# Kernel optimization log

Hardware: AMD Instinct MI355X
Metric: run time of the kernel (lower is better)

## Reference

```python
import jax, jax.numpy as jnp
import numpy as np

H = 32  # hidden_size
D = 512  # input_size


def _lstm_layer(x_tbd, Wih, Whh, b):
    """Single PyTorch-convention LSTM layer.
    x_tbd: [T, B, Din]; Wih: [4H, Din]; Whh: [4H, H]; b: [4H] (b_ih + b_hh).
    Gate order (PyTorch): i, f, g, o. Returns outputs [T, B, H]."""
    T, B, _ = x_tbd.shape
    # Precompute the input contribution for all timesteps at once.
    xg = jnp.einsum('tbd,gd->tbg', x_tbd, Wih) + b  # [T, B, 4H]

    def step(carry, xg_t):
        h, c = carry
        gates = xg_t + h @ Whh.T  # [B, 4H]
        i, f, g, o = jnp.split(gates, 4, axis=-1)
        i = jax.nn.sigmoid(i)
        f = jax.nn.sigmoid(f)
        g = jnp.tanh(g)
        o = jax.nn.sigmoid(o)
        c = f * c + i * g
        h = o * jnp.tanh(c)
        return (h, c), h

    h0 = jnp.zeros((B, H), dtype=x_tbd.dtype)
    c0 = jnp.zeros((B, H), dtype=x_tbd.dtype)
    _, ys = jax.lax.scan(step, (h0, c0), xg)
    return ys  # [T, B, H]


def setup_inputs() -> dict:
    key = jax.random.key(0)
    ks = jax.random.split(key, 9)
    s = 1.0 / np.sqrt(H)  # PyTorch LSTM init: U(-1/sqrt(H), 1/sqrt(H))
    u = lambda k, shape: jax.random.uniform(k, shape, jnp.float32, -s, s)
    return {
        'x': jax.random.normal(ks[0], (64, 1024, D), dtype=jnp.float32),
        'Wih0': u(ks[1], (4 * H, D)),
        'Whh0': u(ks[2], (4 * H, H)),
        'bih0': u(ks[3], (4 * H,)),
        'bhh0': u(ks[4], (4 * H,)),
        'Wih1': u(ks[5], (4 * H, H)),
        'Whh1': u(ks[6], (4 * H, H)),
        'bih1': u(ks[7], (4 * H,)),
        'bhh1': u(ks[8], (4 * H,)),
    }


def reference(x, Wih0, Whh0, bih0, bhh0, Wih1, Whh1, bih1, bhh1):
    # x: [B, T, D] (batch_first) -> scan over time axis
    x_tbd = jnp.transpose(x, (1, 0, 2))  # [T, B, D]
    y0 = _lstm_layer(x_tbd, Wih0, Whh0, bih0 + bhh0)  # [T, B, H]
    y1 = _lstm_layer(y0, Wih1, Whh1, bih1 + bhh1)     # [T, B, H]
    return jnp.transpose(y1, (1, 0, 2))  # [B, T, H]
```

## Files before the change

### kernel.cpp

```cpp
#include <hip/hip_runtime.h>
#include <stdint.h>


#define TT 1024
#define BB 64
#define DD 512
#define HH 32
#define GG 128

typedef _Float16 h2v __attribute__((ext_vector_type(2)));
typedef __fp16 pk2 __attribute__((ext_vector_type(2)));
typedef int int2v __attribute__((ext_vector_type(2)));
typedef _Float16 f16x8 __attribute__((ext_vector_type(8)));
typedef float f32x4 __attribute__((ext_vector_type(4)));

__device__ __forceinline__ uint32_t pack2(float lo, float hi) {
  pk2 p = __builtin_amdgcn_cvt_pkrtz(lo, hi);
  return __builtin_bit_cast(uint32_t, p);
}
__device__ __forceinline__ float dot2(uint32_t a, uint32_t b, float acc) {
  return __builtin_amdgcn_fdot2(__builtin_bit_cast(h2v, a),
                                __builtin_bit_cast(h2v, b), acc, false);
}
__device__ __forceinline__ float fast_rcp(float x) { return __builtin_amdgcn_rcpf(x); }
__device__ __forceinline__ float sigm(float s) { return fast_rcp(1.f + __expf(-s)); }
__device__ __forceinline__ float fast_tanh(float x) {
  return fmaf(2.f, fast_rcp(1.f + __expf(-2.f * x)), -1.f);
}
__device__ __forceinline__ float act_sel(float s, bool ist) {
  float z = ist ? s + s : s;
  float r = fast_rcp(1.f + __expf(-z));
  return ist ? fmaf(2.f, r, -1.f) : r;
}

__device__ __forceinline__ float partner32(float x) {
  int xi = __builtin_bit_cast(int, x);
#if __has_builtin(__builtin_amdgcn_permlane32_swap)
  int2v r = __builtin_amdgcn_permlane32_swap(xi, xi, false, false);
  return __builtin_bit_cast(float, r.x ^ r.y ^ xi);
#else
  int a = xi, b = xi;
  asm("v_permlane32_swap_b32 %0, %1" : "+v"(a), "+v"(b));
  return __builtin_bit_cast(float, a ^ b ^ xi);
#endif
}

__device__ __forceinline__ float xor1_dpp(float x) {
  int xi = __builtin_bit_cast(int, x);
  int r = __builtin_amdgcn_update_dpp(xi, xi, 0xB1, 0xF, 0xF, true);
  return __builtin_bit_cast(float, r);
}

__global__ __launch_bounds__(256) void xg_gemm_mfma(const float* __restrict__ x,
                                                    const float* __restrict__ W,
                                                    const float* __restrict__ bih,
                                                    const float* __restrict__ bhh,
                                                    float* __restrict__ outp) {
  __shared__ _Float16 lxs[128][40];
  __shared__ _Float16 lws[128][40];
  const int tid = threadIdx.x;
  const int m0 = blockIdx.x * 128;
  const int sr = tid >> 1;
  const int sk = (tid & 1) * 16;
  const int w = tid >> 6;
  const int wm = (w >> 1) * 64;
  const int wn = (w & 1) * 64;
  const int lane = tid & 63;
  const int lr = lane & 15;
  const int lk = (lane >> 4) * 8;

  f32x4 acc[4][4];
#pragma unroll
  for (int i = 0; i < 4; ++i)
#pragma unroll
    for (int j = 0; j < 4; ++j) acc[i][j] = (f32x4){0.f, 0.f, 0.f, 0.f};

  for (int k0 = 0; k0 < DD; k0 += 32) {
#pragma unroll
    for (int c = 0; c < 4; ++c) {
      const float4 xv = *(const float4*)(x + (size_t)(m0 + sr) * DD + k0 + sk + c * 4);
      uint2 px;
      px.x = pack2(xv.x, xv.y);
      px.y = pack2(xv.z, xv.w);
      *(uint2*)&lxs[sr][sk + c * 4] = px;
      const float4 wv = *(const float4*)(W + (size_t)sr * DD + k0 + sk + c * 4);
      uint2 pw;
      pw.x = pack2(wv.x, wv.y);
      pw.y = pack2(wv.z, wv.w);
      *(uint2*)&lws[sr][sk + c * 4] = pw;
    }
    __syncthreads();
    f16x8 af[4], bf[4];
#pragma unroll
    for (int s = 0; s < 4; ++s) {
      af[s] = *(const f16x8*)&lxs[wm + s * 16 + lr][lk];
      bf[s] = *(const f16x8*)&lws[wn + s * 16 + lr][lk];
    }
#pragma unroll
    for (int mi = 0; mi < 4; ++mi)
#pragma unroll
      for (int ni = 0; ni < 4; ++ni)
        acc[mi][ni] = __builtin_amdgcn_mfma_f32_16x16x32_f16(af[mi], bf[ni],
                                                             acc[mi][ni], 0, 0, 0);
    __syncthreads();
  }
  const int rq = (lane >> 4) * 4;
#pragma unroll
  for (int ni = 0; ni < 4; ++ni) {
    const int g = wn + ni * 16 + lr;
    const float bsum = bih[g] + bhh[g];
#pragma unroll
    for (int mi = 0; mi < 4; ++mi) {
      const int mbase = m0 + wm + mi * 16 + rq;
#pragma unroll
      for (int q = 0; q < 4; ++q)
        outp[(size_t)(mbase + q) * GG + g] = acc[mi][ni][q] + bsum;
    }
  }
}

__global__ __launch_bounds__(64)
__attribute__((amdgpu_waves_per_eu(1)))
void lstm_scan(const float* __restrict__ xg,
               const float* __restrict__ Whh0,
               const float* __restrict__ Wih1,
               const float* __restrict__ Whh1,
               const float* __restrict__ bih1,
               const float* __restrict__ bhh1,
               float* __restrict__ out) {
  const int l = threadIdx.x;
  const int j = l & 31;
  const int hi = l >> 5;
  const int b = blockIdx.x;
  const int gA = j + 64 * hi;
  const int gB = gA + 32;

  uint32_t w0A[16], w0B[16], wiA[16], whA[16], wiB[16], whB[16];
#pragma unroll
  for (int q = 0; q < 8; ++q) {
    float4 a = *(const float4*)(Whh0 + (size_t)gA * HH + q * 4);
    float4 c = *(const float4*)(Whh0 + (size_t)gB * HH + q * 4);
    w0A[2 * q] = pack2(a.x, a.y); w0A[2 * q + 1] = pack2(a.z, a.w);
    w0B[2 * q] = pack2(c.x, c.y); w0B[2 * q + 1] = pack2(c.z, c.w);
    float4 d = *(const float4*)(Wih1 + (size_t)gA * HH + q * 4);
    float4 e = *(const float4*)(Wih1 + (size_t)gB * HH + q * 4);
    wiA[2 * q] = pack2(d.x, d.y); wiA[2 * q + 1] = pack2(d.z, d.w);
    wiB[2 * q] = pack2(e.x, e.y); wiB[2 * q + 1] = pack2(e.z, e.w);
    float4 f = *(const float4*)(Whh1 + (size_t)gA * HH + q * 4);
    float4 g = *(const float4*)(Whh1 + (size_t)gB * HH + q * 4);
    whA[2 * q] = pack2(f.x, f.y); whA[2 * q + 1] = pack2(f.z, f.w);
    whB[2 * q] = pack2(g.x, g.y); whB[2 * q + 1] = pack2(g.z, g.w);
  }
#pragma unroll
  for (int k = 0; k < 16; ++k) {
    asm volatile("" : "+v"(w0A[k]));
    asm volatile("" : "+v"(w0B[k]));
    asm volatile("" : "+v"(wiA[k]));
    asm volatile("" : "+v"(wiB[k]));
    asm volatile("" : "+v"(whA[k]));
    asm volatile("" : "+v"(whB[k]));
  }
  const float b1A = bih1[gA] + bhh1[gA];
  const float b1B = bih1[gB] + bhh1[gB];

  uint32_t h0p[16], h1p[16];
#pragma unroll
  for (int k = 0; k < 16; ++k) { h0p[k] = 0u; h1p[k] = 0u; }
  float c0 = 0.f, c1 = 0.f;

  const float* xgp = xg + (size_t)b * TT * GG;
  float* outp = out + (size_t)b * TT * HH;

  float xA[4], xB[4];
#pragma unroll
  for (int u = 0; u < 4; ++u) {
    xA[u] = xgp[u * GG + gA];
    xB[u] = xgp[u * GG + gB];
  }

  for (int tb = 0; tb < TT; tb += 4) {
#pragma unroll
    for (int u = 0; u < 4; ++u) {
      const int t = tb + u;
      float sA0 = xA[u], sB0 = xB[u];
      const int tp = (t + 4 < TT) ? (t + 4) : (TT - 1);
      xA[u] = xgp[(size_t)tp * GG + gA];
      xB[u] = xgp[(size_t)tp * GG + gB];
      float pA = 0.f, pB = 0.f;
#pragma unroll
      for (int k = 0; k < 16; k += 2) {
        sA0 = dot2(w0A[k], h0p[k], sA0);
        pA  = dot2(w0A[k + 1], h0p[k + 1], pA);
        sB0 = dot2(w0B[k], h0p[k], sB0);
        pB  = dot2(w0B[k + 1], h0p[k + 1], pB);
      }
      sA0 += pA; sB0 += pB;
      float sA1 = b1A, sB1 = b1B, qA = 0.f, qB = 0.f;
#pragma unroll
      for (int k = 0; k < 16; k += 2) {
        sA1 = dot2(wiA[k], h0p[k], sA1);
        qA  = dot2(wiA[k + 1], h0p[k + 1], qA);
        sB1 = dot2(wiB[k], h0p[k], sB1);
        qB  = dot2(wiB[k + 1], h0p[k + 1], qB);
        sA1 = dot2(whA[k], h1p[k], sA1);
        qA  = dot2(whA[k + 1], h1p[k + 1], qA);
        sB1 = dot2(whB[k], h1p[k], sB1);
        qB  = dot2(whB[k + 1], h1p[k + 1], qB);
      }
      sA1 += qA; sB1 += qB;
      {
        float aA = act_sel(sA0, hi != 0);
        float aB = sigm(sB0);
        float pAx = partner32(aA);
        float pBx = partner32(aB);
        float gi = hi ? pAx : aA;
        float gf = hi ? pBx : aB;
        float gg = hi ? aA : pAx;
        float go = hi ? aB : pBx;
        c0 = fmaf(gf, c0, gi * gg);
        float h = go * fast_tanh(c0);
        float oth = xor1_dpp(h);
        float lo = (j & 1) ? oth : h;
        float hh = (j & 1) ? h : oth;
        uint32_t pk = pack2(lo, hh);
#pragma unroll
        for (int m = 0; m < 16; ++m)
          h0p[m] = (uint32_t)__builtin_amdgcn_readlane((int)pk, 2 * m);
      }
      if (t > 0) {
        float aA = act_sel(sA1, hi != 0);
        float aB = sigm(sB1);
        float pAx = partner32(aA);
        float pBx = partner32(aB);
        float gi = hi ? pAx : aA;
        float gf = hi ? pBx : aB;
        float gg = hi ? aA : pAx;
        float go = hi ? aB : pBx;
        c1 = fmaf(gf, c1, gi * gg);
        float h = go * fast_tanh(c1);
        if (!hi) outp[(size_t)(t - 1) * HH + j] = h;
        float oth = xor1_dpp(h);
        float lo = (j & 1) ? oth : h;
        float hh = (j & 1) ? h : oth;
        uint32_t pk = pack2(lo, hh);
#pragma unroll
        for (int m = 0; m < 16; ++m)
          h1p[m] = (uint32_t)__builtin_amdgcn_readlane((int)pk, 2 * m);
      }
    }
  }
  {
    float sA1 = b1A, sB1 = b1B, qA = 0.f, qB = 0.f;
#pragma unroll
    for (int k = 0; k < 16; k += 2) {
      sA1 = dot2(wiA[k], h0p[k], sA1);
      qA  = dot2(wiA[k + 1], h0p[k + 1], qA);
      sB1 = dot2(wiB[k], h0p[k], sB1);
      qB  = dot2(wiB[k + 1], h0p[k + 1], qB);
      sA1 = dot2(whA[k], h1p[k], sA1);
      qA  = dot2(whA[k + 1], h1p[k + 1], qA);
      sB1 = dot2(whB[k], h1p[k], sB1);
      qB  = dot2(whB[k + 1], h1p[k + 1], qB);
    }
    sA1 += qA; sB1 += qB;
    float aA = act_sel(sA1, hi != 0);
    float aB = sigm(sB1);
    float pAx = partner32(aA);
    float pBx = partner32(aB);
    float gi = hi ? pAx : aA;
    float gf = hi ? pBx : aB;
    float gg = hi ? aA : pAx;
    float go = hi ? aB : pBx;
    c1 = fmaf(gf, c1, gi * gg);
    float h = go * fast_tanh(c1);
    if (!hi) outp[(size_t)(TT - 1) * HH + j] = h;
  }
}

extern "C" void kernel_launch(void* const* d_in, const int* in_sizes, int n_in,
                              void* d_out, int out_size, void* d_ws, size_t ws_size,
                              hipStream_t stream) {
  const float* x = (const float*)d_in[0];
  const float* Wih0 = (const float*)d_in[1];
  const float* Whh0 = (const float*)d_in[2];
  const float* bih0 = (const float*)d_in[3];
  const float* bhh0 = (const float*)d_in[4];
  const float* Wih1 = (const float*)d_in[5];
  const float* Whh1 = (const float*)d_in[6];
  const float* bih1 = (const float*)d_in[7];
  const float* bhh1 = (const float*)d_in[8];
  float* out = (float*)d_out;
  float* xg = (float*)d_ws;

  xg_gemm_mfma<<<dim3((BB * TT) / 128), dim3(256), 0, stream>>>(x, Wih0, bih0, bhh0, xg);
  lstm_scan<<<dim3(BB), dim3(64), 0, stream>>>(xg, Whh0, Wih1, Whh1, bih1, bhh1, out);
}
```

Measured before the change: 497.2 us.

## Split LSTM layers into producer/consumer waves with an LDS ring buffer

The single-wave recurrent scan is split across two wavefronts per block. Wave 0 runs layer 0 and precomputes part of layer 1's input projection. Wave 1 runs layer 1, reading h0 and the partial sums from a shared-memory ring buffer, with spin-wait counters for flow control. The aim is to overlap the two layers' serial dependency chains so each per-step critical path gets shorter. This adds LDS traffic, polling with s_sleep, and relies on volatile counters plus a block fence for memory ordering.

```diff
diff --git a/kernel.cpp b/kernel.cpp
--- a/kernel.cpp
+++ b/kernel.cpp
@@ -7,6 +7,7 @@
 #define DD 512
 #define HH 32
 #define GG 128
+#define RINGD 8
 
 typedef _Float16 h2v __attribute__((ext_vector_type(2)));
 typedef __fp16 pk2 __attribute__((ext_vector_type(2)));
@@ -119,96 +120,80 @@
   }
 }
 
-__global__ __launch_bounds__(64)
-__attribute__((amdgpu_waves_per_eu(1)))
-void lstm_scan(const float* __restrict__ xg,
-               const float* __restrict__ Whh0,
-               const float* __restrict__ Wih1,
-               const float* __restrict__ Whh1,
-               const float* __restrict__ bih1,
-               const float* __restrict__ bhh1,
-               float* __restrict__ out) {
-  const int l = threadIdx.x;
+__global__ __launch_bounds__(128)
+void lstm_scan2(const float* __restrict__ xg,
+                const float* __restrict__ Whh0,
+                const float* __restrict__ Wih1,
+                const float* __restrict__ Whh1,
+                const float* __restrict__ bih1,
+                const float* __restrict__ bhh1,
+                float* __restrict__ out) {
+  __shared__ alignas(16) uint32_t h0ring[RINGD][16];
+  __shared__ alignas(16) float pring[RINGD][64];
+  __shared__ volatile int prodCnt;
+  __shared__ volatile int consCnt;
+
+  const int tid = threadIdx.x;
+  const int wid = tid >> 6;
+  const int l = tid & 63;
   const int j = l & 31;
   const int hi = l >> 5;
   const int b = blockIdx.x;
   const int gA = j + 64 * hi;
   const int gB = gA + 32;
 
-  uint32_t w0A[16], w0B[16], wiA[16], whA[16], wiB[16], whB[16];
-#pragma unroll
-  for (int q = 0; q < 8; ++q) {
-    float4 a = *(const float4*)(Whh0 + (size_t)gA * HH + q * 4);
-    float4 c = *(const float4*)(Whh0 + (size_t)gB * HH + q * 4);
-    w0A[2 * q] = pack2(a.x, a.y); w0A[2 * q + 1] = pack2(a.z, a.w);
-    w0B[2 * q] = pack2(c.x, c.y); w0B[2 * q + 1] = pack2(c.z, c.w);
-    float4 d = *(const float4*)(Wih1 + (size_t)gA * HH + q * 4);
-    float4 e = *(const float4*)(Wih1 + (size_t)gB * HH + q * 4);
-    wiA[2 * q] = pack2(d.x, d.y); wiA[2 * q + 1] = pack2(d.z, d.w);
-    wiB[2 * q] = pack2(e.x, e.y); wiB[2 * q + 1] = pack2(e.z, e.w);
-    float4 f = *(const float4*)(Whh1 + (size_t)gA * HH + q * 4);
-    float4 g = *(const float4*)(Whh1 + (size_t)gB * HH + q * 4);
-    whA[2 * q] = pack2(f.x, f.y); whA[2 * q + 1] = pack2(f.z, f.w);
-    whB[2 * q] = pack2(g.x, g.y); whB[2 * q + 1] = pack2(g.z, g.w);
-  }
-#pragma unroll
-  for (int k = 0; k < 16; ++k) {
-    asm volatile("" : "+v"(w0A[k]));
-    asm volatile("" : "+v"(w0B[k]));
-    asm volatile("" : "+v"(wiA[k]));
-    asm volatile("" : "+v"(wiB[k]));
-    asm volatile("" : "+v"(whA[k]));
-    asm volatile("" : "+v"(whB[k]));
-  }
-  const float b1A = bih1[gA] + bhh1[gA];
-  const float b1B = bih1[gB] + bhh1[gB];
-
-  uint32_t h0p[16], h1p[16];
-#pragma unroll
-  for (int k = 0; k < 16; ++k) { h0p[k] = 0u; h1p[k] = 0u; }
-  float c0 = 0.f, c1 = 0.f;
-
-  const float* xgp = xg + (size_t)b * TT * GG;
-  float* outp = out + (size_t)b * TT * HH;
-
-  float xA[4], xB[4];
-#pragma unroll
-  for (int u = 0; u < 4; ++u) {
-    xA[u] = xgp[u * GG + gA];
-    xB[u] = xgp[u * GG + gB];
-  }
-
-  for (int tb = 0; tb < TT; tb += 4) {
+  if (tid == 0) { prodCnt = 0; consCnt = 0; }
+  __syncthreads();
+
+  if (wid == 0) {
+    uint32_t w0A[16], w0B[16], wiA[16];
+#pragma unroll
+    for (int q = 0; q < 8; ++q) {
+      float4 a = *(const float4*)(Whh0 + (size_t)gA * HH + q * 4);
+      float4 c = *(const float4*)(Whh0 + (size_t)gB * HH + q * 4);
+      w0A[2 * q] = pack2(a.x, a.y); w0A[2 * q + 1] = pack2(a.z, a.w);
+      w0B[2 * q] = pack2(c.x, c.y); w0B[2 * q + 1] = pack2(c.z, c.w);
+      float4 d = *(const float4*)(Wih1 + (size_t)gA * HH + q * 4);
+      wiA[2 * q] = pack2(d.x, d.y); wiA[2 * q + 1] = pack2(d.z, d.w);
+    }
+    uint32_t h0p[16];
+#pragma unroll
+    for (int k = 0; k < 16; ++k) h0p[k] = 0u;
+    float c0 = 0.f;
+
+    const float* xgp = xg + (size_t)b * TT * GG;
+    float xA[4], xB[4];
 #pragma unroll
     for (int u = 0; u < 4; ++u) {
-      const int t = tb + u;
-      float sA0 = xA[u], sB0 = xB[u];
-      const int tp = (t + 4 < TT) ? (t + 4) : (TT - 1);
-      xA[u] = xgp[(size_t)tp * GG + gA];
-      xB[u] = xgp[(size_t)tp * GG + gB];
-      float pA = 0.f, pB = 0.f;
-#pragma unroll
-      for (int k = 0; k < 16; k += 2) {
-        sA0 = dot2(w0A[k], h0p[k], sA0);
-        pA  = dot2(w0A[k + 1], h0p[k + 1], pA);
-        sB0 = dot2(w0B[k], h0p[k], sB0);
-        pB  = dot2(w0B[k + 1], h0p[k + 1], pB);
-      }
-      sA0 += pA; sB0 += pB;
-      float sA1 = b1A, sB1 = b1B, qA = 0.f, qB = 0.f;
-#pragma unroll
-      for (int k = 0; k < 16; k += 2) {
-        sA1 = dot2(wiA[k], h0p[k], sA1);
-        qA  = dot2(wiA[k + 1], h0p[k + 1], qA);
-        sB1 = dot2(wiB[k], h0p[k], sB1);
-        qB  = dot2(wiB[k + 1], h0p[k + 1], qB);
-        sA1 = dot2(whA[k], h1p[k], sA1);
-        qA  = dot2(whA[k + 1], h1p[k + 1], qA);
-        sB1 = dot2(whB[k], h1p[k], sB1);
-        qB  = dot2(whB[k + 1], h1p[k + 1], qB);
-      }
-      sA1 += qA; sB1 += qB;
-      {
+      xA[u] = xgp[u * GG + gA];
+      xB[u] = xgp[u * GG + gB];
+    }
+    const bool wrt = (!hi) && ((j & 1) == 0);
+    int cachedCons = 0;
+
+    for (int tb = 0; tb < TT; tb += 4) {
+#pragma unroll
+      for (int u = 0; u < 4; ++u) {
+        const int t = tb + u;
+        if (t - cachedCons >= RINGD) {
+          do {
+            __builtin_amdgcn_s_sleep(1);
+            cachedCons = consCnt;
+          } while (t - cachedCons >= RINGD);
+        }
+        float sA0 = xA[u], sB0 = xB[u];
+        const int tp = (t + 4 < TT) ? (t + 4) : (TT - 1);
+        xA[u] = xgp[(size_t)tp * GG + gA];
+        xB[u] = xgp[(size_t)tp * GG + gB];
+        float pA = 0.f, pB = 0.f;
+#pragma unroll
+        for (int k = 0; k < 16; k += 2) {
+          sA0 = dot2(w0A[k], h0p[k], sA0);
+          pA  = dot2(w0A[k + 1], h0p[k + 1], pA);
+          sB0 = dot2(w0B[k], h0p[k], sB0);
+          pB  = dot2(w0B[k + 1], h0p[k + 1], pB);
+        }
+        sA0 += pA; sB0 += pB;
         float aA = act_sel(sA0, hi != 0);
         float aB = sigm(sB0);
         float pAx = partner32(aA);
@@ -226,54 +211,87 @@
 #pragma unroll
         for (int m = 0; m < 16; ++m)
           h0p[m] = (uint32_t)__builtin_amdgcn_readlane((int)pk, 2 * m);
+        float pp0 = 0.f, pp1 = 0.f;
+#pragma unroll
+        for (int k = 0; k < 16; k += 2) {
+          pp0 = dot2(wiA[k], h0p[k], pp0);
+          pp1 = dot2(wiA[k + 1], h0p[k + 1], pp1);
+        }
+        if (wrt) h0ring[t & (RINGD - 1)][j >> 1] = pk;
+        pring[t & (RINGD - 1)][l] = pp0 + pp1;
+        __threadfence_block();
+        if (l == 0) prodCnt = t + 1;
       }
-      if (t > 0) {
-        float aA = act_sel(sA1, hi != 0);
-        float aB = sigm(sB1);
-        float pAx = partner32(aA);
-        float pBx = partner32(aB);
-        float gi = hi ? pAx : aA;
-        float gf = hi ? pBx : aB;
-        float gg = hi ? aA : pAx;
-        float go = hi ? aB : pBx;
-        c1 = fmaf(gf, c1, gi * gg);
-        float h = go * fast_tanh(c1);
-        if (!hi) outp[(size_t)(t - 1) * HH + j] = h;
-        float oth = xor1_dpp(h);
-        float lo = (j & 1) ? oth : h;
-        float hh = (j & 1) ? h : oth;
-        uint32_t pk = pack2(lo, hh);
-#pragma unroll
-        for (int m = 0; m < 16; ++m)
-          h1p[m] = (uint32_t)__builtin_amdgcn_readlane((int)pk, 2 * m);
+    }
+  } else {
+    uint32_t wiB[16], whA[16], whB[16];
+#pragma unroll
+    for (int q = 0; q < 8; ++q) {
+      float4 e = *(const float4*)(Wih1 + (size_t)gB * HH + q * 4);
+      wiB[2 * q] = pack2(e.x, e.y); wiB[2 * q + 1] = pack2(e.z, e.w);
+      float4 f = *(const float4*)(Whh1 + (size_t)gA * HH + q * 4);
+      float4 g = *(const float4*)(Whh1 + (size_t)gB * HH + q * 4);
+      whA[2 * q] = pack2(f.x, f.y); whA[2 * q + 1] = pack2(f.z, f.w);
+      whB[2 * q] = pack2(g.x, g.y); whB[2 * q + 1] = pack2(g.z, g.w);
+    }
+    const float b1A = bih1[gA] + bhh1[gA];
+    const float b1B = bih1[gB] + bhh1[gB];
+
+    uint32_t h1p[16];
+#pragma unroll
+    for (int k = 0; k < 16; ++k) h1p[k] = 0u;
+    float c1 = 0.f;
+    float* outp = out + (size_t)b * TT * HH;
+    int cachedProd = 0;
+
+    for (int t = 0; t < TT; ++t) {
+      if (cachedProd <= t) {
+        do {
+          __builtin_amdgcn_s_sleep(1);
+          cachedProd = prodCnt;
+        } while (cachedProd <= t);
       }
-    }
-  }
-  {
-    float sA1 = b1A, sB1 = b1B, qA = 0.f, qB = 0.f;
-#pragma unroll
-    for (int k = 0; k < 16; k += 2) {
-      sA1 = dot2(wiA[k], h0p[k], sA1);
-      qA  = dot2(wiA[k + 1], h0p[k + 1], qA);
-      sB1 = dot2(wiB[k], h0p[k], sB1);
-      qB  = dot2(wiB[k + 1], h0p[k + 1], qB);
-      sA1 = dot2(whA[k], h1p[k], sA1);
-      qA  = dot2(whA[k + 1], h1p[k + 1], qA);
-      sB1 = dot2(whB[k], h1p[k], sB1);
-      qB  = dot2(whB[k + 1], h1p[k + 1], qB);
-    }
-    sA1 += qA; sB1 += qB;
-    float aA = act_sel(sA1, hi != 0);
-    float aB = sigm(sB1);
-    float pAx = partner32(aA);
-    float pBx = partner32(aB);
-    float gi = hi ? pAx : aA;
-    float gf = hi ? pBx : aB;
-    float gg = hi ? aA : pAx;
-    float go = hi ? aB : pBx;
-    c1 = fmaf(gf, c1, gi * gg);
-    float h = go * fast_tanh(c1);
-    if (!hi) outp[(size_t)(TT - 1) * HH + j] = h;
+      asm volatile("" ::: "memory");
+      const uint32_t* hrow = &h0ring[t & (RINGD - 1)][0];
+      uint4 r0 = ((const uint4*)hrow)[0];
+      uint4 r1 = ((const uint4*)hrow)[1];
+      uint4 r2 = ((const uint4*)hrow)[2];
+      uint4 r3 = ((const uint4*)hrow)[3];
+      uint32_t h0v[16] = {r0.x, r0.y, r0.z, r0.w, r1.x, r1.y, r1.z, r1.w,
+                          r2.x, r2.y, r2.z, r2.w, r3.x, r3.y, r3.z, r3.w};
+      const float pp = pring[t & (RINGD - 1)][l];
+      float sA1 = b1A + pp, sB1 = b1B, qA = 0.f, qB = 0.f;
+#pragma unroll
+      for (int k = 0; k < 16; k += 2) {
+        sA1 = dot2(whA[k], h1p[k], sA1);
+        qA  = dot2(whA[k + 1], h1p[k + 1], qA);
+        sB1 = dot2(wiB[k], h0v[k], sB1);
+        qB  = dot2(wiB[k + 1], h0v[k + 1], qB);
+        sB1 = dot2(whB[k], h1p[k], sB1);
+        qB  = dot2(whB[k + 1], h1p[k + 1], qB);
+      }
+      sA1 += qA; sB1 += qB;
+      float aA = act_sel(sA1, hi != 0);
+      float aB = sigm(sB1);
+      float pAx = partner32(aA);
+      float pBx = partner32(aB);
+      float gi = hi ? pAx : aA;
+      float gf = hi ? pBx : aB;
+      float gg = hi ? aA : pAx;
+      float go = hi ? aB : pBx;
+      c1 = fmaf(gf, c1, gi * gg);
+      float h = go * fast_tanh(c1);
+      if (!hi) outp[(size_t)t * HH + j] = h;
+      float oth = xor1_dpp(h);
+      float lo = (j & 1) ? oth : h;
+      float hh = (j & 1) ? h : oth;
+      uint32_t pk = pack2(lo, hh);
+#pragma unroll
+      for (int m = 0; m < 16; ++m)
+        h1p[m] = (uint32_t)__builtin_amdgcn_readlane((int)pk, 2 * m);
+      asm volatile("" ::: "memory");
+      if (l == 0) consCnt = t + 1;
+    }
   }
 }
 
@@ -293,5 +311,5 @@
   float* xg = (float*)d_ws;
 
   xg_gemm_mfma<<<dim3((BB * TT) / 128), dim3(256), 0, stream>>>(x, Wih0, bih0, bhh0, xg);
-  lstm_scan<<<dim3(BB), dim3(64), 0, stream>>>(xg, Whh0, Wih1, Whh1, bih1, bhh1, out);
-}
+  lstm_scan2<<<dim3(BB), dim3(128), 0, stream>>>(xg, Whh0, Wih1, Whh1, bih1, bhh1, out);
+}
```

Result: slower. 533.0 us (+7.2%).
